# Kernel tuning notes

Hardware: AMD Instinct MI355X
Metric: run time of the kernel (lower is better)

The kernel has to match this reference:

```python
import jax, jax.numpy as jnp
import numpy as np

N = 50000
F_IN = 256
D_HID = 64
H = 8
C = 10
E_RAND = 800000
ALPHA = 0.2  # leaky_relu negative slope


def setup_inputs() -> dict:
    key = jax.random.key(0)
    k = jax.random.split(key, 7)
    x = jax.random.normal(k[0], (N, F_IN), dtype=jnp.float32)
    # edge list = self-loops (ensure nonzero softmax denominator) + random edges
    self_idx = jnp.arange(N, dtype=jnp.int32)
    edge_src = jnp.concatenate([self_idx, jax.random.randint(k[1], (E_RAND,), 0, N, dtype=jnp.int32)])
    edge_dst = jnp.concatenate([self_idx, jax.random.randint(k[2], (E_RAND,), 0, N, dtype=jnp.int32)])
    W_heads = jax.random.normal(k[3], (H, F_IN, D_HID), dtype=jnp.float32) * 0.05
    a_heads = jax.random.normal(k[4], (H, 2 * D_HID), dtype=jnp.float32) * 0.05
    W_out = jax.random.normal(k[5], (H * D_HID, C), dtype=jnp.float32) * 0.05
    a_out = jax.random.normal(k[6], (2 * C,), dtype=jnp.float32) * 0.05
    return {"x": x, "edge_src": edge_src, "edge_dst": edge_dst,
            "W_heads": W_heads, "a_heads": a_heads, "W_out": W_out, "a_out": a_out}


def sp_gat_layer(x, W, a, src, dst, concat):
    """pyGAT SpGraphAttentionLayer (eval mode, dropout off)."""
    n = x.shape[0]
    d = W.shape[1]
    h = x @ W                                             # [N, d]
    score = h[src] @ a[:d] + h[dst] @ a[d:]               # [E] per-edge attention logit
    e = jnp.exp(-jax.nn.leaky_relu(score, ALPHA))         # unnormalized attention
    rowsum = jax.ops.segment_sum(e, src, num_segments=n)  # [N] softmax denominator
    agg = jax.ops.segment_sum(e[:, None] * h[dst], src, num_segments=n)  # [N, d]
    out = agg / rowsum[:, None]
    return jax.nn.elu(out) if concat else out


def reference(x, edge_src, edge_dst, W_heads, a_heads, W_out, a_out):
    # multi-head sparse attention, heads concatenated along feature dim
    heads = jax.vmap(lambda W, a: sp_gat_layer(x, W, a, edge_src, edge_dst, True))(W_heads, a_heads)  # [H, N, d]
    xcat = jnp.transpose(heads, (1, 0, 2)).reshape(x.shape[0], -1)  # [N, H*d]
    out = jax.nn.elu(sp_gat_layer(xcat, W_out, a_out, edge_src, edge_dst, False))  # [N, C]
    return jax.nn.log_softmax(out, axis=1)
```

## Files before the change

### kernel.cpp

```cpp
#include <hip/hip_runtime.h>
#include <hip/hip_bf16.h>

#define F_IN    256
#define D_HID   64
#define H_HEADS 8
#define NC      10
#define ALPHA   0.2f
#define SCAN_T  1024

typedef __attribute__((ext_vector_type(8))) short short8;
typedef __attribute__((ext_vector_type(4))) float f32x4;

__device__ __forceinline__ float bfu2f(unsigned short u) {
    union { float f; unsigned int i; } c; c.i = ((unsigned int)u) << 16; return c.f;
}
__device__ __forceinline__ unsigned short f2bfu(float f) {
    union { float f; unsigned int i; } c; c.f = f;
    unsigned int x = c.i;
    x += 0x7fffu + ((x >> 16) & 1u);
    return (unsigned short)(x >> 16);
}

__device__ __forceinline__ bool detect_f32(const void* xraw) {
    unsigned int w = ((const unsigned int*)xraw)[threadIdx.x & 63];
    unsigned int e = (w >> 7) & 0xffu;
    unsigned long long m = __ballot(e >= 140u);
    return __popcll(m) > 8;
}

__global__ __launch_bounds__(256) void prep_kernel(
    const void* __restrict__ x_raw,  unsigned short* __restrict__ x_bf,
    const void* __restrict__ Wh_raw, unsigned short* __restrict__ wh_f,
    const void* __restrict__ ah_raw, float* __restrict__ ah32,
    const void* __restrict__ Wo_raw, float* __restrict__ Wo32,
    const void* __restrict__ ao_raw, float* __restrict__ ao32,
    const int* __restrict__ esrc, int* __restrict__ counts,
    int N, int E, int bx, int bw, int ba, int bo)
{
    int b = blockIdx.x;
    bool isf32 = detect_f32(x_raw);
    if (b < bx) {
        long i = (long)b * 256 + threadIdx.x;
        long n8 = (long)N * F_IN / 8;
        if (i < n8) {
            unsigned short o[8];
            if (isf32) {
                const float* s = (const float*)x_raw + i * 8;
                #pragma unroll
                for (int j = 0; j < 8; ++j) o[j] = f2bfu(s[j]);
            } else {
                *(uint4*)o = ((const uint4*)x_raw)[i];
            }
            *(uint4*)(x_bf + i * 8) = *(uint4*)o;
        }
    } else if (b < bw) {
        int i = (b - bx) * 256 + threadIdx.x;
        int d = i & 63, k = (i >> 6) & 255, h = i >> 14;
        float v = isf32 ? ((const float*)Wh_raw)[i] : bfu2f(((const unsigned short*)Wh_raw)[i]);
        int ks = k >> 5, q = (k >> 3) & 3, j = k & 7;
        int c = d >> 4, m = d & 15;
        wh_f[(((h * 8 + ks) * 4 + c) << 9) + (q * 16 + m) * 8 + j] = f2bfu(v);
    } else if (b < ba) {
        int i = (b - bw) * 256 + threadIdx.x;
        ah32[i] = isf32 ? ((const float*)ah_raw)[i] : bfu2f(((const unsigned short*)ah_raw)[i]);
    } else if (b < bo) {
        int i = (b - ba) * 256 + threadIdx.x;
        Wo32[i] = isf32 ? ((const float*)Wo_raw)[i] : bfu2f(((const unsigned short*)Wo_raw)[i]);
    } else if (b == bo) {
        int i = threadIdx.x;
        if (i < 2 * NC)
            ao32[i] = isf32 ? ((const float*)ao_raw)[i] : bfu2f(((const unsigned short*)ao_raw)[i]);
    } else {
        int e = (b - bo - 1) * 256 + threadIdx.x;
        if (e < E) atomicAdd(&counts[esrc[e]], 1);
    }
}

__global__ __launch_bounds__(SCAN_T) void scan_kernel(
    const int* __restrict__ counts, int* __restrict__ row_start, int N, int E)
{
    __shared__ int sums[SCAN_T];
    int t = threadIdx.x;
    int chunk = (N + SCAN_T - 1) / SCAN_T;
    int b = t * chunk, e = min(b + chunk, N);
    int s = 0;
    for (int i = b; i < e; ++i) s += counts[i];
    sums[t] = s;
    __syncthreads();
    for (int off = 1; off < SCAN_T; off <<= 1) {
        int u = (t >= off) ? sums[t - off] : 0;
        __syncthreads();
        sums[t] += u;
        __syncthreads();
    }
    int running = sums[t] - s;
    for (int i = b; i < e; ++i) { row_start[i] = running; running += counts[i]; }
    if (t == SCAN_T - 1) row_start[N] = E;
}

__global__ __launch_bounds__(256) void scatter_ev_kernel(
    const int* __restrict__ src, const int* __restrict__ dst,
    const int* __restrict__ row_start, int* __restrict__ cursor,
    const float* __restrict__ s1s, const float* __restrict__ s1d,
    int* __restrict__ csr_dst, float* __restrict__ ev_csr, int E)
{
    int e = blockIdx.x * 256 + threadIdx.x;
    if (e >= E) return;
    int s = src[e], d = dst[e];
    int pos = atomicAdd(&cursor[s], 1);
    int i = row_start[s] + pos;
    csr_dst[i] = d;
    float4 ss0 = *(const float4*)(s1s + s * 8);
    float4 ss1 = *(const float4*)(s1s + s * 8 + 4);
    float4 sd0 = *(const float4*)(s1d + d * 8);
    float4 sd1 = *(const float4*)(s1d + d * 8 + 4);
    float sc[8] = { ss0.x + sd0.x, ss0.y + sd0.y, ss0.z + sd0.z, ss0.w + sd0.w,
                    ss1.x + sd1.x, ss1.y + sd1.y, ss1.z + sd1.z, ss1.w + sd1.w };
    float ev[8];
    #pragma unroll
    for (int h = 0; h < 8; ++h) {
        float lr = sc[h] > 0.f ? sc[h] : ALPHA * sc[h];
        ev[h] = __expf(-lr);
    }
    *(float4*)(ev_csr + (long)i * 8)     = make_float4(ev[0], ev[1], ev[2], ev[3]);
    *(float4*)(ev_csr + (long)i * 8 + 4) = make_float4(ev[4], ev[5], ev[6], ev[7]);
}

__global__ __launch_bounds__(256) void gemm1_kernel(
    const unsigned short* __restrict__ x_bf,
    const unsigned short* __restrict__ wh_f,
    const float* __restrict__ ah,
    unsigned short* __restrict__ h_bf,
    float* __restrict__ s1s, float* __restrict__ s1d, int N)
{
    __shared__ unsigned short Os[64][72];

    const int t = threadIdx.x;
    const int w = t >> 6, lane = t & 63;
    const int q = lane >> 4, m = lane & 15;
    const int n0 = blockIdx.x * 64;
    const int h0 = blockIdx.y * 2;

    int r = n0 + 16 * w + m;
    const unsigned short* xr = x_bf + (long)(r < N ? r : N - 1) * 256;
    short8 afrag[8];
    #pragma unroll
    for (int ks = 0; ks < 8; ++ks)
        afrag[ks] = *(const short8*)(xr + ks * 32 + q * 8);

    #pragma unroll
    for (int hi = 0; hi < 2; ++hi) {
        const int h = h0 + hi;
        f32x4 acc[4] = {};
        const unsigned short* Bh = wh_f + (((long)h * 32) << 9);
        #pragma unroll
        for (int ks = 0; ks < 8; ++ks) {
            #pragma unroll
            for (int c = 0; c < 4; ++c) {
                short8 b = *(const short8*)(Bh + (((ks * 4 + c) << 9) + lane * 8));
                acc[c] = __builtin_amdgcn_mfma_f32_16x16x32_bf16(afrag[ks], b, acc[c], 0, 0, 0);
            }
        }

        const float* a1 = ah + h * 128;
        float a1m = a1[m], a1m16 = a1[16 + m], a1m32 = a1[32 + m], a1m48 = a1[48 + m];
        float a2m = a1[64 + m], a2m16 = a1[80 + m], a2m32 = a1[96 + m], a2m48 = a1[112 + m];
        #pragma unroll
        for (int reg = 0; reg < 4; ++reg) {
            float p1 = acc[0][reg] * a1m + acc[1][reg] * a1m16 + acc[2][reg] * a1m32 + acc[3][reg] * a1m48;
            float p2 = acc[0][reg] * a2m + acc[1][reg] * a2m16 + acc[2][reg] * a2m32 + acc[3][reg] * a2m48;
            #pragma unroll
            for (int off = 1; off < 16; off <<= 1) {
                p1 += __shfl_xor(p1, off);
                p2 += __shfl_xor(p2, off);
            }
            int row = n0 + 16 * w + q * 4 + reg;
            if (m == 0 && row < N) {
                s1s[row * 8 + h] = p1;
                s1d[row * 8 + h] = p2;
            }
        }

        #pragma unroll
        for (int c = 0; c < 4; ++c)
            #pragma unroll
            for (int reg = 0; reg < 4; ++reg)
                Os[16 * w + q * 4 + reg][c * 16 + m] = f2bfu(acc[c][reg]);
        #pragma unroll
        for (int j = 0; j < 2; ++j) {
            int cc = j * 64 + lane;
            int row = cc >> 3, c8 = cc & 7;
            if (n0 + 16 * w + row < N)
                *(uint4*)(h_bf + (long)(n0 + 16 * w + row) * 512 + h * 64 + c8 * 8) =
                    *(const uint4*)&Os[16 * w + row][c8 * 8];
        }
    }
}

__global__ __launch_bounds__(256) void edge_agg1_kernel(
    const int* __restrict__ row_start, const int* __restrict__ csr_dst,
    const float* __restrict__ ev_csr,
    const uint4* __restrict__ h_q,
    uint4* __restrict__ xcat_q,
    int N)
{
    int lane = threadIdx.x & 63;
    int n = blockIdx.x * 4 + (threadIdx.x >> 6);
    if (n >= N) return;
    int h = lane >> 3;
    int beg = row_start[n], end = row_start[n + 1];

    float acc[8] = {0.f, 0.f, 0.f, 0.f, 0.f, 0.f, 0.f, 0.f};
    float rs = 0.f;
    int dnext = csr_dst[beg];
    for (int i = beg; i < end; ++i) {
        int d = dnext;
        if (i + 1 < end) dnext = csr_dst[i + 1];
        float ev = ev_csr[(long)i * 8 + h];
        uint4 wv = h_q[(long)d * 64 + lane];
        rs += ev;
        acc[0] += ev * bfu2f((unsigned short)(wv.x & 0xffffu));
        acc[1] += ev * bfu2f((unsigned short)(wv.x >> 16));
        acc[2] += ev * bfu2f((unsigned short)(wv.y & 0xffffu));
        acc[3] += ev * bfu2f((unsigned short)(wv.y >> 16));
        acc[4] += ev * bfu2f((unsigned short)(wv.z & 0xffffu));
        acc[5] += ev * bfu2f((unsigned short)(wv.z >> 16));
        acc[6] += ev * bfu2f((unsigned short)(wv.w & 0xffffu));
        acc[7] += ev * bfu2f((unsigned short)(wv.w >> 16));
    }
    float inv = 1.f / rs;
    unsigned short o[8];
    #pragma unroll
    for (int j = 0; j < 8; ++j) {
        float v = acc[j] * inv;
        v = v > 0.f ? v : __expf(v) - 1.f;
        o[j] = f2bfu(v);
    }
    xcat_q[(long)n * 64 + lane] = *(const uint4*)o;
}

__global__ __launch_bounds__(256) void gemm2_kernel(
    const unsigned short* __restrict__ xcat_bf,
    const float* __restrict__ Wo,
    const float* __restrict__ ao,
    float* __restrict__ h2p,
    float* __restrict__ s2s, float* __restrict__ s2d, int N)
{
    int tid = blockIdx.x * 256 + threadIdx.x;
    int n = tid >> 1;
    if (n >= N) return;
    int half = tid & 1;
    float acc[NC];
    #pragma unroll
    for (int c = 0; c < NC; ++c) acc[c] = 0.f;
    const uint4* xp = (const uint4*)(xcat_bf + (long)n * 512) + half * 32;
    for (int k8 = 0; k8 < 32; ++k8) {
        uint4 w = xp[k8];
        float f[8];
        f[0] = bfu2f((unsigned short)(w.x & 0xffffu)); f[1] = bfu2f((unsigned short)(w.x >> 16));
        f[2] = bfu2f((unsigned short)(w.y & 0xffffu)); f[3] = bfu2f((unsigned short)(w.y >> 16));
        f[4] = bfu2f((unsigned short)(w.z & 0xffffu)); f[5] = bfu2f((unsigned short)(w.z >> 16));
        f[6] = bfu2f((unsigned short)(w.w & 0xffffu)); f[7] = bfu2f((unsigned short)(w.w >> 16));
        #pragma unroll
        for (int u = 0; u < 8; ++u) {
            const float* wr = Wo + ((half * 32 + k8) * 8 + u) * NC;
            #pragma unroll
            for (int c = 0; c < NC; ++c) acc[c] += f[u] * wr[c];
        }
    }
    #pragma unroll
    for (int c = 0; c < NC; ++c) acc[c] += __shfl_xor(acc[c], 1, 64);
    if (half == 0) {
        float s1 = 0.f, s2 = 0.f;
        *(float4*)(h2p + (long)n * 16)      = make_float4(acc[0], acc[1], acc[2], acc[3]);
        *(float4*)(h2p + (long)n * 16 + 4)  = make_float4(acc[4], acc[5], acc[6], acc[7]);
        *(float4*)(h2p + (long)n * 16 + 8)  = make_float4(acc[8], acc[9], 0.f, 0.f);
        *(float4*)(h2p + (long)n * 16 + 12) = make_float4(0.f, 0.f, 0.f, 0.f);
        #pragma unroll
        for (int c = 0; c < NC; ++c) {
            s1 += acc[c] * ao[c];
            s2 += acc[c] * ao[NC + c];
        }
        s2s[n] = s1;
        s2d[n] = s2;
    }
}

__global__ __launch_bounds__(256) void edge_agg2_kernel(
    const int* __restrict__ row_start, const int* __restrict__ csr_dst,
    const float* __restrict__ h2p,
    const float* __restrict__ s_src2, const float* __restrict__ s_dst2,
    void* __restrict__ out, const void* __restrict__ x_raw, int N)
{
    bool isf32 = detect_f32(x_raw);
    int lane = threadIdx.x & 63;
    int n = blockIdx.x * 4 + (threadIdx.x >> 6);
    if (n >= N) return;
    int c = lane & 15, j = lane >> 4;
    int beg = row_start[n], end = row_start[n + 1];
    float ss = s_src2[n];
    float rs = 0.f, acc = 0.f;
    for (int i0 = beg; i0 < end; i0 += 4) {
        int i = i0 + j;
        if (i < end) {
            int d = csr_dst[i];
            float sc = ss + s_dst2[d];
            float lr = sc > 0.f ? sc : ALPHA * sc;
            float ev = __expf(-lr);
            rs += ev;
            acc += ev * h2p[(long)d * 16 + c];
        }
    }
    rs  += __shfl_xor(rs, 16, 64);  rs  += __shfl_xor(rs, 32, 64);
    acc += __shfl_xor(acc, 16, 64); acc += __shfl_xor(acc, 32, 64);
    float v = acc / rs;
    v = v > 0.f ? v : __expf(v) - 1.f;
    float vm = (c < NC) ? v : -1e30f;
    #pragma unroll
    for (int off = 1; off < 16; off <<= 1) vm = fmaxf(vm, __shfl_xor(vm, off, 64));
    float ex = (c < NC) ? __expf(v - vm) : 0.f;
    #pragma unroll
    for (int off = 1; off < 16; off <<= 1) ex += __shfl_xor(ex, off, 64);
    float lse = vm + logf(ex);
    if (c < NC && j == 0) {
        if (isf32) ((float*)out)[(long)n * NC + c] = v - lse;
        else       ((unsigned short*)out)[(long)n * NC + c] = f2bfu(v - lse);
    }
}

extern "C" void kernel_launch(void* const* d_in, const int* in_sizes, int n_in,
                              void* d_out, int out_size, void* d_ws, size_t ws_size,
                              hipStream_t stream)
{
    const void* x_raw  = d_in[0];
    const int*  esrc   = (const int*)d_in[1];
    const int*  edst   = (const int*)d_in[2];
    const void* Wh_raw = d_in[3];
    const void* ah_raw = d_in[4];
    const void* Wo_raw = d_in[5];
    const void* ao_raw = d_in[6];

    const int N = in_sizes[0] / F_IN;
    const int E = in_sizes[1];

    char* ws = (char*)d_ws;
    size_t off = 0;
    auto alloc = [&](size_t bytes) -> void* {
        void* p = ws + off;
        off = (off + bytes + 255) & ~(size_t)255;
        return p;
    };
    int*            counts    = (int*)           alloc((size_t)N * 4);
    int*            cursor    = (int*)           alloc((size_t)N * 4);
    size_t clear_span = (size_t)((char*)cursor + (size_t)N * 4 - (char*)counts);

    unsigned short* x_bf      = (unsigned short*)alloc((size_t)N * F_IN * 2);
    unsigned short* wh_f      = (unsigned short*)alloc((size_t)H_HEADS * D_HID * F_IN * 2);
    float*          ah32      = (float*)         alloc((size_t)H_HEADS * 2 * D_HID * 4);
    float*          Wo32      = (float*)         alloc((size_t)512 * NC * 4);
    float*          ao32      = (float*)         alloc((size_t)2 * NC * 4);
    unsigned short* h_bf      = (unsigned short*)alloc((size_t)N * 512 * 2);
    unsigned short* xcat_bf   = (unsigned short*)alloc((size_t)N * 512 * 2);
    float*          s1s       = (float*)         alloc((size_t)N * 8 * 4);
    float*          s1d       = (float*)         alloc((size_t)N * 8 * 4);
    float*          h2p       = (float*)         alloc((size_t)N * 16 * 4);
    float*          s2s       = (float*)         alloc((size_t)N * 4);
    float*          s2d       = (float*)         alloc((size_t)N * 4);
    int*            row_start = (int*)           alloc((size_t)(N + 1) * 4);
    int*            csr_dst   = (int*)           alloc((size_t)E * 4);
    float*          ev_csr    = (float*)         alloc((size_t)E * 8 * 4);
    (void)ws_size;

    hipMemsetAsync(counts, 0, clear_span, stream);

    int bx = (int)(((long)N * F_IN / 8 + 255) / 256);
    int bw = bx + (H_HEADS * F_IN * D_HID) / 256;
    int ba = bw + (H_HEADS * 2 * D_HID) / 256;
    int bo = ba + (512 * NC) / 256;
    int nb = bo + 1 + (E + 255) / 256;
    prep_kernel<<<nb, 256, 0, stream>>>(x_raw, x_bf, Wh_raw, wh_f, ah_raw, ah32,
                                        Wo_raw, Wo32, ao_raw, ao32,
                                        esrc, counts, N, E, bx, bw, ba, bo);
    scan_kernel<<<1, SCAN_T, 0, stream>>>(counts, row_start, N, E);

    dim3 g1((N + 63) / 64, H_HEADS / 2);
    gemm1_kernel<<<g1, 256, 0, stream>>>(x_bf, wh_f, ah32, h_bf, s1s, s1d, N);
    scatter_ev_kernel<<<(E + 255) / 256, 256, 0, stream>>>(esrc, edst, row_start, cursor,
                                                           s1s, s1d, csr_dst, ev_csr, E);
    edge_agg1_kernel<<<(N + 3) / 4, 256, 0, stream>>>(row_start, csr_dst, ev_csr,
                                                      (const uint4*)h_bf, (uint4*)xcat_bf, N);

    gemm2_kernel<<<(2 * N + 255) / 256, 256, 0, stream>>>(xcat_bf, Wo32, ao32, h2p, s2s, s2d, N);
    edge_agg2_kernel<<<(N + 3) / 4, 256, 0, stream>>>(row_start, csr_dst, h2p, s2s, s2d, d_out, x_raw, N);
}
```

Before: 561.1 us.

## Compute edge attention weights inside aggregation instead of materialising per-edge buffer

```diff
diff --git a/kernel.cpp b/kernel.cpp
--- a/kernel.cpp
+++ b/kernel.cpp
@@ -45,9 +45,12 @@
         if (i < n8) {
             unsigned short o[8];
             if (isf32) {
-                const float* s = (const float*)x_raw + i * 8;
-                #pragma unroll
-                for (int j = 0; j < 8; ++j) o[j] = f2bfu(s[j]);
+                const float4* s = (const float4*)x_raw + i * 2;
+                float4 a = s[0], bb = s[1];
+                o[0] = f2bfu(a.x);  o[1] = f2bfu(a.y);
+                o[2] = f2bfu(a.z);  o[3] = f2bfu(a.w);
+                o[4] = f2bfu(bb.x); o[5] = f2bfu(bb.y);
+                o[6] = f2bfu(bb.z); o[7] = f2bfu(bb.w);
             } else {
                 *(uint4*)o = ((const uint4*)x_raw)[i];
             }
@@ -98,32 +101,16 @@
     if (t == SCAN_T - 1) row_start[N] = E;
 }
 
-__global__ __launch_bounds__(256) void scatter_ev_kernel(
+__global__ __launch_bounds__(256) void scatter_kernel(
     const int* __restrict__ src, const int* __restrict__ dst,
     const int* __restrict__ row_start, int* __restrict__ cursor,
-    const float* __restrict__ s1s, const float* __restrict__ s1d,
-    int* __restrict__ csr_dst, float* __restrict__ ev_csr, int E)
+    int* __restrict__ csr_dst, int E)
 {
     int e = blockIdx.x * 256 + threadIdx.x;
     if (e >= E) return;
-    int s = src[e], d = dst[e];
+    int s = src[e];
     int pos = atomicAdd(&cursor[s], 1);
-    int i = row_start[s] + pos;
-    csr_dst[i] = d;
-    float4 ss0 = *(const float4*)(s1s + s * 8);
-    float4 ss1 = *(const float4*)(s1s + s * 8 + 4);
-    float4 sd0 = *(const float4*)(s1d + d * 8);
-    float4 sd1 = *(const float4*)(s1d + d * 8 + 4);
-    float sc[8] = { ss0.x + sd0.x, ss0.y + sd0.y, ss0.z + sd0.z, ss0.w + sd0.w,
-                    ss1.x + sd1.x, ss1.y + sd1.y, ss1.z + sd1.z, ss1.w + sd1.w };
-    float ev[8];
-    #pragma unroll
-    for (int h = 0; h < 8; ++h) {
-        float lr = sc[h] > 0.f ? sc[h] : ALPHA * sc[h];
-        ev[h] = __expf(-lr);
-    }
-    *(float4*)(ev_csr + (long)i * 8)     = make_float4(ev[0], ev[1], ev[2], ev[3]);
-    *(float4*)(ev_csr + (long)i * 8 + 4) = make_float4(ev[4], ev[5], ev[6], ev[7]);
+    csr_dst[row_start[s] + pos] = dst[e];
 }
 
 __global__ __launch_bounds__(256) void gemm1_kernel(
@@ -199,7 +186,7 @@
 
 __global__ __launch_bounds__(256) void edge_agg1_kernel(
     const int* __restrict__ row_start, const int* __restrict__ csr_dst,
-    const float* __restrict__ ev_csr,
+    const float* __restrict__ s1s, const float* __restrict__ s1d,
     const uint4* __restrict__ h_q,
     uint4* __restrict__ xcat_q,
     int N)
@@ -209,15 +196,38 @@
     if (n >= N) return;
     int h = lane >> 3;
     int beg = row_start[n], end = row_start[n + 1];
+    float ss = s1s[n * 8 + h];
 
     float acc[8] = {0.f, 0.f, 0.f, 0.f, 0.f, 0.f, 0.f, 0.f};
     float rs = 0.f;
-    int dnext = csr_dst[beg];
-    for (int i = beg; i < end; ++i) {
-        int d = dnext;
-        if (i + 1 < end) dnext = csr_dst[i + 1];
-        float ev = ev_csr[(long)i * 8 + h];
+    int i = beg;
+    for (; i + 2 <= end; i += 2) {
+        int d0 = csr_dst[i], d1 = csr_dst[i + 1];
+        float sd0 = s1d[d0 * 8 + h];
+        float sd1 = s1d[d1 * 8 + h];
+        uint4 w0 = h_q[(long)d0 * 64 + lane];
+        uint4 w1 = h_q[(long)d1 * 64 + lane];
+        float sc0 = ss + sd0, sc1 = ss + sd1;
+        float lr0 = sc0 > 0.f ? sc0 : ALPHA * sc0;
+        float lr1 = sc1 > 0.f ? sc1 : ALPHA * sc1;
+        float ev0 = __expf(-lr0), ev1 = __expf(-lr1);
+        rs += ev0 + ev1;
+        acc[0] += ev0 * bfu2f((unsigned short)(w0.x & 0xffffu)) + ev1 * bfu2f((unsigned short)(w1.x & 0xffffu));
+        acc[1] += ev0 * bfu2f((unsigned short)(w0.x >> 16))     + ev1 * bfu2f((unsigned short)(w1.x >> 16));
+        acc[2] += ev0 * bfu2f((unsigned short)(w0.y & 0xffffu)) + ev1 * bfu2f((unsigned short)(w1.y & 0xffffu));
+        acc[3] += ev0 * bfu2f((unsigned short)(w0.y >> 16))     + ev1 * bfu2f((unsigned short)(w1.y >> 16));
+        acc[4] += ev0 * bfu2f((unsigned short)(w0.z & 0xffffu)) + ev1 * bfu2f((unsigned short)(w1.z & 0xffffu));
+        acc[5] += ev0 * bfu2f((unsigned short)(w0.z >> 16))     + ev1 * bfu2f((unsigned short)(w1.z >> 16));
+        acc[6] += ev0 * bfu2f((unsigned short)(w0.w & 0xffffu)) + ev1 * bfu2f((unsigned short)(w1.w & 0xffffu));
+        acc[7] += ev0 * bfu2f((unsigned short)(w0.w >> 16))     + ev1 * bfu2f((unsigned short)(w1.w >> 16));
+    }
+    if (i < end) {
+        int d = csr_dst[i];
+        float sd = s1d[d * 8 + h];
         uint4 wv = h_q[(long)d * 64 + lane];
+        float sc = ss + sd;
+        float lr = sc > 0.f ? sc : ALPHA * sc;
+        float ev = __expf(-lr);
         rs += ev;
         acc[0] += ev * bfu2f((unsigned short)(wv.x & 0xffffu));
         acc[1] += ev * bfu2f((unsigned short)(wv.x >> 16));
@@ -368,7 +378,6 @@
     float*          s2d       = (float*)         alloc((size_t)N * 4);
     int*            row_start = (int*)           alloc((size_t)(N + 1) * 4);
     int*            csr_dst   = (int*)           alloc((size_t)E * 4);
-    float*          ev_csr    = (float*)         alloc((size_t)E * 8 * 4);
     (void)ws_size;
 
     hipMemsetAsync(counts, 0, clear_span, stream);
@@ -382,12 +391,11 @@
                                         Wo_raw, Wo32, ao_raw, ao32,
                                         esrc, counts, N, E, bx, bw, ba, bo);
     scan_kernel<<<1, SCAN_T, 0, stream>>>(counts, row_start, N, E);
+    scatter_kernel<<<(E + 255) / 256, 256, 0, stream>>>(esrc, edst, row_start, cursor, csr_dst, E);
 
     dim3 g1((N + 63) / 64, H_HEADS / 2);
     gemm1_kernel<<<g1, 256, 0, stream>>>(x_bf, wh_f, ah32, h_bf, s1s, s1d, N);
-    scatter_ev_kernel<<<(E + 255) / 256, 256, 0, stream>>>(esrc, edst, row_start, cursor,
-                                                           s1s, s1d, csr_dst, ev_csr, E);
-    edge_agg1_kernel<<<(N + 3) / 4, 256, 0, stream>>>(row_start, csr_dst, ev_csr,
+    edge_agg1_kernel<<<(N + 3) / 4, 256, 0, stream>>>(row_start, csr_dst, s1s, s1d,
                                                       (const uint4*)h_bf, (uint4*)xcat_bf, N);
 
     gemm2_kernel<<<(2 * N + 255) / 256, 256, 0, stream>>>(xcat_bf, Wo32, ao32, h2p, s2s, s2d, N);
```

Measured after the change: 542.9 us. 1.03x faster.
